# Kernel tuning notes

Measured on AMD Instinct MI355X. Metric: run time of the kernel, lower is better.

The kernel has to match this reference:

```python
import jax, jax.numpy as jnp
import numpy as np

H, L, NH, DH, FF, V, MAXP = 768, 2, 12, 64, 3072, 50265, 512
B, S = 64, 512


def _ln(x, g, b, eps=1e-5):
    mu = jnp.mean(x, axis=-1, keepdims=True)
    var = jnp.mean(jnp.square(x - mu), axis=-1, keepdims=True)
    return (x - mu) * jax.lax.rsqrt(var + eps) * g + b


def setup_inputs() -> dict:
    key = jax.random.key(0)
    ks = jax.random.split(key, 16)
    sd = 0.02
    inp = {
        "source_ids": jax.random.randint(ks[0], (B, S), 0, V),
        "position_idx": jax.random.randint(ks[1], (B, S), 0, MAXP),
        "attn_mask": jax.random.randint(ks[2], (B, S, S), 0, 2).astype(bool),
        "word_emb": sd * jax.random.normal(ks[3], (V, H), jnp.float32),
        "pos_emb": sd * jax.random.normal(ks[4], (MAXP, H), jnp.float32),
        "ln_g": jnp.ones((H,), jnp.float32),
        "ln_b": jnp.zeros((H,), jnp.float32),
        "Wqkv": sd * jax.random.normal(ks[5], (L, H, 3 * H), jnp.float32),
        "bqkv": jnp.zeros((L, 3 * H), jnp.float32),
        "Wo": sd * jax.random.normal(ks[6], (L, H, H), jnp.float32),
        "bo": jnp.zeros((L, H), jnp.float32),
        "ln1_g": jnp.ones((L, H), jnp.float32),
        "ln1_b": jnp.zeros((L, H), jnp.float32),
        "W1": sd * jax.random.normal(ks[7], (L, H, FF), jnp.float32),
        "b1": jnp.zeros((L, FF), jnp.float32),
        "W2": sd * jax.random.normal(ks[8], (L, FF, H), jnp.float32),
        "b2": jnp.zeros((L, H), jnp.float32),
        "ln2_g": jnp.ones((L, H), jnp.float32),
        "ln2_b": jnp.zeros((L, H), jnp.float32),
        "dense_W": sd * jax.random.normal(ks[9], (H, H), jnp.float32),
        "dense_b": jnp.zeros((H,), jnp.float32),
        "out_W": sd * jax.random.normal(ks[10], (H, 1), jnp.float32),
        "out_b": jnp.zeros((1,), jnp.float32),
    }
    return inp


def reference(source_ids, position_idx, attn_mask, word_emb, pos_emb, ln_g, ln_b,
              Wqkv, bqkv, Wo, bo, ln1_g, ln1_b, W1, b1, W2, b2, ln2_g, ln2_b,
              dense_W, dense_b, out_W, out_b):
    nodes_mask = position_idx == 0          # [B,S] bool
    token_mask = position_idx >= 2          # [B,S] bool
    emb = word_emb[source_ids]              # [B,S,H]

    # node -> token masked mean aggregation (the custom-kernel hotspot)
    m = (nodes_mask[:, :, None] & token_mask[:, None, :] & attn_mask).astype(emb.dtype)  # [B,S,S]
    w = m / (jnp.sum(m, axis=-1, keepdims=True) + 1e-10)
    avg = jnp.einsum('bnt,btd->bnd', w, emb)
    nm = nodes_mask[:, :, None].astype(emb.dtype)
    emb = emb * (1.0 - nm) + avg * nm

    # RoBERTa-style embeddings: inputs_embeds + position embeddings, layernorm
    h = _ln(emb + pos_emb[position_idx], ln_g, ln_b)

    # additive attention bias from 3D mask
    bias = jnp.where(attn_mask, 0.0, -1e4).astype(h.dtype)[:, None, :, :]  # [B,1,S,S]
    scale = 1.0 / np.sqrt(DH)

    for l in range(L):
        qkv = h @ Wqkv[l] + bqkv[l]                     # [B,S,3H]
        q, k, v = jnp.split(qkv, 3, axis=-1)
        q = q.reshape(B, S, NH, DH)
        k = k.reshape(B, S, NH, DH)
        v = v.reshape(B, S, NH, DH)
        scores = jnp.einsum('bqhd,bkhd->bhqk', q, k) * scale + bias
        attn = jax.nn.softmax(scores, axis=-1)
        ctx = jnp.einsum('bhqk,bkhd->bqhd', attn, v).reshape(B, S, H)
        h = _ln(h + ctx @ Wo[l] + bo[l], ln1_g[l], ln1_b[l])
        ffn = jax.nn.gelu(h @ W1[l] + b1[l], approximate=False) @ W2[l] + b2[l]
        h = _ln(h + ffn, ln2_g[l], ln2_b[l])

    # classification head (dropout in eval = identity)
    x = h[:, 0, :]
    x = jnp.tanh(x @ dense_W + dense_b)
    logits = x @ out_W + out_b                          # [B,1]
    return logits
```

## Files before the change

kernel.cpp:

```cpp
#include <hip/hip_runtime.h>

typedef unsigned short u16;
typedef unsigned int   u32;
typedef __bf16 bf16x8 __attribute__((ext_vector_type(8)));
typedef float  f32x4  __attribute__((ext_vector_type(4)));

#define DEVI __device__ __forceinline__

DEVI u16 f2bf(float f){
  u32 u = __builtin_bit_cast(u32, f);
  u32 r = (u + 0x7fffu + ((u >> 16) & 1u)) >> 16;
  return (u16)r;
}
DEVI float bf2f(u16 u){
  u32 x = ((u32)u) << 16;
  return __builtin_bit_cast(float, x);
}

DEVI void gload16(const void* g, void* lds){
  __builtin_amdgcn_global_load_lds(
      (const __attribute__((address_space(1))) void*)g,
      (__attribute__((address_space(3))) void*)lds, 16, 0, 0);
}

DEVI f32x4 MFMA(bf16x8 a, bf16x8 b, f32x4 c){
  return __builtin_amdgcn_mfma_f32_16x16x32_bf16(a, b, c, 0, 0, 0);
}

#define BAR() do { asm volatile("s_barrier" ::: "memory"); \
                   __builtin_amdgcn_sched_barrier(0); } while(0)

__global__ void k_maskprobe(const unsigned char* __restrict__ m, int* __restrict__ flag){
  __shared__ int s;
  if (threadIdx.x == 0) s = 0;
  __syncthreads();
  int acc = 0;
  for (int i = threadIdx.x; i < 65536; i += 256)
    if ((i & 3) != 0 && m[i] != 0) acc++;
  atomicAdd(&s, acc);
  __syncthreads();
  if (threadIdx.x == 0) *flag = (s > 0) ? 1 : 0;
}

__global__ void k_maskbits(const void* __restrict__ mask, const int* __restrict__ flag,
                           u32* __restrict__ mb){
  int row  = blockIdx.x * 4 + (threadIdx.x >> 6);
  int lane = threadIdx.x & 63;
  bool bytes = (*flag != 0);
  for (int c0 = 0; c0 < 512; c0 += 64){
    int v;
    if (bytes) v = ((const unsigned char*)mask)[(size_t)row * 512 + c0 + lane];
    else       v = ((const int*)mask)[(size_t)row * 512 + c0 + lane];
    unsigned long long bits = __ballot(v != 0);
    if (lane == 0){
      mb[(size_t)row * 16 + (c0 >> 5)]     = (u32)(bits & 0xffffffffull);
      mb[(size_t)row * 16 + (c0 >> 5) + 1] = (u32)(bits >> 32);
    }
  }
}

__global__ void k_embln(const int* __restrict__ ids, const int* __restrict__ pos,
                        const u32* __restrict__ mb, const float* __restrict__ wemb,
                        const float* __restrict__ pemb, const float* __restrict__ g,
                        const float* __restrict__ be, u16* __restrict__ hb){
  __shared__ float s1[4], s2[4];
  int row = blockIdx.x, t = threadIdx.x;
  int p = pos[row];
  float x0, x1, x2;
  if (p == 0){
    int b = row >> 9;
    const u32* mrow = mb + (size_t)row * 16;
    const int* pb = pos + ((size_t)b << 9);
    const int* ib = ids + ((size_t)b << 9);
    float a0 = 0.f, a1 = 0.f, a2 = 0.f, cnt = 0.f;
    #pragma unroll 8
    for (int k = 0; k < 512; k++){
      float w = (pb[k] >= 2 && ((mrow[k >> 5] >> (k & 31)) & 1)) ? 1.f : 0.f;
      const float* src = wemb + (size_t)ib[k] * 768;
      a0 += w * src[t]; a1 += w * src[t+256]; a2 += w * src[t+512];
      cnt += w;
    }
    float inv = 1.f / (cnt + 1e-10f);
    x0 = a0 * inv; x1 = a1 * inv; x2 = a2 * inv;
  } else {
    const float* src = wemb + (size_t)ids[row] * 768;
    x0 = src[t]; x1 = src[t+256]; x2 = src[t+512];
  }
  const float* pr = pemb + (size_t)p * 768;
  x0 += pr[t]; x1 += pr[t+256]; x2 += pr[t+512];
  float s = x0 + x1 + x2, q = x0*x0 + x1*x1 + x2*x2;
  for (int o = 32; o; o >>= 1){ s += __shfl_down(s, o, 64); q += __shfl_down(q, o, 64); }
  int wv = t >> 6, ln = t & 63;
  if (!ln){ s1[wv] = s; s2[wv] = q; }
  __syncthreads();
  s = s1[0]+s1[1]+s1[2]+s1[3]; q = s2[0]+s2[1]+s2[2]+s2[3];
  float mu = s * (1.f/768.f);
  float rs = rsqrtf(q * (1.f/768.f) - mu*mu + 1e-5f);
  u16* hbr = hb + (size_t)row * 768;
  hbr[t]     = f2bf((x0-mu)*rs*g[t]     + be[t]);
  hbr[t+256] = f2bf((x1-mu)*rs*g[t+256] + be[t+256]);
  hbr[t+512] = f2bf((x2-mu)*rs*g[t+512] + be[t+512]);
}

__global__ void k_lnres(const u16* __restrict__ C, const float* __restrict__ g,
                        const float* __restrict__ be, u16* __restrict__ hb){
  __shared__ float s1[4], s2[4];
  int row = blockIdx.x, t = threadIdx.x;
  u16* hr = hb + (size_t)row * 768;
  const u16* cr = C + (size_t)row * 768;
  float x0 = bf2f(hr[t])     + bf2f(cr[t]);
  float x1 = bf2f(hr[t+256]) + bf2f(cr[t+256]);
  float x2 = bf2f(hr[t+512]) + bf2f(cr[t+512]);
  float s = x0 + x1 + x2, q = x0*x0 + x1*x1 + x2*x2;
  for (int o = 32; o; o >>= 1){ s += __shfl_down(s, o, 64); q += __shfl_down(q, o, 64); }
  int wv = t >> 6, ln = t & 63;
  if (!ln){ s1[wv] = s; s2[wv] = q; }
  __syncthreads();
  s = s1[0]+s1[1]+s1[2]+s1[3]; q = s2[0]+s2[1]+s2[2]+s2[3];
  float mu = s * (1.f/768.f);
  float rs = rsqrtf(q * (1.f/768.f) - mu*mu + 1e-5f);
  hr[t]     = f2bf((x0-mu)*rs*g[t]     + be[t]);
  hr[t+256] = f2bf((x1-mu)*rs*g[t+256] + be[t+256]);
  hr[t+512] = f2bf((x2-mu)*rs*g[t+512] + be[t+512]);
}

__global__ void k_transpose(const float* __restrict__ src, u16* __restrict__ dst,
                            int K, int N){
  __shared__ float tile[32][33];
  int k0 = blockIdx.x * 32, n0 = blockIdx.y * 32;
  int tx = threadIdx.x & 31, ty = threadIdx.x >> 5;
  #pragma unroll
  for (int i = 0; i < 32; i += 8)
    tile[ty + i][tx] = src[(size_t)(k0 + ty + i) * N + n0 + tx];
  __syncthreads();
  #pragma unroll
  for (int i = 0; i < 32; i += 8)
    dst[(size_t)(n0 + ty + i) * K + k0 + tx] = f2bf(tile[tx][ty + i]);
}


DEVI void stageA32(const u16* __restrict__ src, int K, u16* lds, int tid){
  int r = tid >> 2, c = tid & 3;
  int sc = c ^ ((r >> 1) & 3);
  gload16(src + (size_t)r*K + sc*8, lds + (size_t)tid*8);
}
DEVI void stageB32(const u16* __restrict__ src, int K, u16* lds, int tid){
  #pragma unroll
  for (int j = 0; j < 2; j++){
    int p = j*512 + tid;
    int r = p >> 2, c = p & 3;
    int sc = c ^ ((r >> 1) & 3);
    gload16(src + (size_t)r*K + sc*8, lds + (size_t)p*8);
  }
}

template<int EPI>
__global__ __launch_bounds__(512, 4)
void k_gemm3(const u16* __restrict__ A, const u16* __restrict__ BT,
             const float* __restrict__ bias, void* __restrict__ out,
             void* __restrict__ out2, int M, int N, int K){
  __shared__ __align__(16) u16 sm[36864];
  const int tid = threadIdx.x;
  const int w = tid >> 6, lane = tid & 63;
  const int wm = w >> 2, wn = w & 3;
  const int cr = lane & 15, cg = lane >> 4;

  const int nbn = gridDim.x;
  const int nwg = nbn * gridDim.y;
  const int d   = blockIdx.y * nbn + blockIdx.x;
  const int xcd = d & 7, qq = nwg >> 3, rr = nwg & 7;
  const int logical = (xcd < rr ? xcd*(qq+1) : rr*(qq+1) + (xcd-rr)*qq) + (d >> 3);
  const int m0 = (logical / nbn) * 128;
  const int n0 = (logical % nbn) * 256;

  const int NT = K >> 5;
  const u16* Abase = A  + (size_t)m0 * K;
  const u16* Bbase = BT + (size_t)n0 * K;
  const int rowA = wm*64 + cr;
  const int rowB = wn*64 + cr;

  f32x4 acc[4][4] = {};
  bf16x8 afr[4], bfr[4];

  stageA32(Abase, K, sm, tid);
  stageB32(Bbase, K, sm + 12288, tid);
  if (NT > 1){
    stageA32(Abase + 32, K, sm + 4096, tid);
    stageB32(Bbase + 32, K, sm + 12288 + 8192, tid);
    asm volatile("s_waitcnt vmcnt(3)" ::: "memory");
  } else {
    asm volatile("s_waitcnt vmcnt(0)" ::: "memory");
  }
  __builtin_amdgcn_sched_barrier(0);
  BAR();

  int bcur = 0;
  for (int t = 0; t < NT; ++t){
    const int ab = bcur << 12;
    const int bb = 12288 + (bcur << 13);
    int bn2 = bcur + 2; if (bn2 >= 3) bn2 -= 3;

    #pragma unroll
    for (int n = 0; n < 4; n++){
      int r = rowB + n*16;
      bfr[n] = *(const bf16x8*)&sm[bb + r*32 + ((cg ^ ((r >> 1) & 3)) << 3)];
    }
    #pragma unroll
    for (int i = 0; i < 4; i++){
      int r = rowA + i*16;
      afr[i] = *(const bf16x8*)&sm[ab + r*32 + ((cg ^ ((r >> 1) & 3)) << 3)];
    }
    if (t + 2 < NT){
      stageA32(Abase + (size_t)(t+2)*32, K, sm + (bn2 << 12), tid);
      stageB32(Bbase + (size_t)(t+2)*32, K, sm + 12288 + (bn2 << 13), tid);
    }

    __builtin_amdgcn_s_setprio(1);
    #pragma unroll
    for (int i = 0; i < 4; i++)
      #pragma unroll
      for (int n = 0; n < 4; n++)
        acc[i][n] = MFMA(afr[i], bfr[n], acc[i][n]);
    __builtin_amdgcn_s_setprio(0);

    if (t + 2 < NT) { asm volatile("s_waitcnt vmcnt(3)" ::: "memory"); }
    else            { asm volatile("s_waitcnt vmcnt(0)" ::: "memory"); }
    __builtin_amdgcn_sched_barrier(0);
    BAR();
    bcur = bcur + 1; if (bcur >= 3) bcur = 0;
  }

  if (EPI == 1){
    #pragma unroll
    for (int n = 0; n < 4; n++){
      int col = n0 + wn*64 + n*16 + cr;
      float bv = bias[col];
      #pragma unroll
      for (int i = 0; i < 4; i++){
        #pragma unroll
        for (int j = 0; j < 4; j++){
          int row = m0 + wm*64 + i*16 + cg*4 + j;
          ((float*)out)[(size_t)row * N + col] = acc[i][n][j] + bv;
        }
      }
    }
  } else {
    const bool vblk = (EPI == 3) && (n0 >= 1536);
    const int LDC = vblk ? 266 : 264;
    #pragma unroll
    for (int n = 0; n < 4; n++){
      int coll = wn*64 + n*16 + cr;
      float bv = bias[n0 + coll];
      #pragma unroll
      for (int i = 0; i < 4; i++){
        #pragma unroll
        for (int j = 0; j < 4; j++){
          int rowl = wm*64 + i*16 + cg*4 + j;
          float v = acc[i][n][j] + bv;
          if (EPI == 2) v = 0.5f * v * (1.f + erff(v * 0.70710678118654752f));
          sm[rowl*LDC + coll] = f2bf(v);
        }
      }
    }
    BAR();
    if (EPI == 3){
      int b = m0 >> 9, s0 = m0 & 511;
      if (vblk){
        int hd0 = (n0 - 1536) >> 6;
        int dl = lane >> 2, sc4 = lane & 3;
        #pragma unroll
        for (int it = 0; it < 8; it++){
          int gidx = it*8 + w;
          int hh2 = gidx >> 4, dhi = (gidx >> 2) & 3, shi = gidx & 3;
          int dd2 = dhi*16 + dl;
          int schunk = shi*4 + sc4;
          u16 tmp[8];
          #pragma unroll
          for (int k = 0; k < 8; k++)
            tmp[k] = sm[(schunk*8 + k)*266 + hh2*64 + dd2];
          *(uint4*)((u16*)out2 + (((size_t)(b*12 + hd0 + hh2)*64 + dd2) << 9)
                    + s0 + schunk*8) = *(uint4*)tmp;
        }
      } else {
        #pragma unroll
        for (int it = 0; it < 8; it++){
          int idx = it*512 + tid;
          int c = idx & 7, hh2 = (idx >> 3) & 3, s = idx >> 5;
          uint4 v4 = *(const uint4*)&sm[s*264 + hh2*64 + c*8];
          int col0 = n0 + hh2*64;
          int sec = (col0 >= 768) ? 1 : 0;
          int hd  = (col0 - sec*768) >> 6;
          *(uint4*)((u16*)out + (size_t)sec*25165824 +
                    (((size_t)(b*12 + hd)*512 + (m0 & 511) + s) << 6) + c*8) = v4;
        }
      }
    } else {
      #pragma unroll
      for (int it = 0; it < 8; it++){
        int idx = it*512 + tid;
        int r = idx >> 5, c8 = idx & 31;
        uint4 v4 = *(const uint4*)&sm[r*264 + c8*8];
        *(uint4*)((u16*)out + (size_t)(m0 + r)*N + n0 + c8*8) = v4;
      }
    }
  }
}

DEVI void stage64(const u16* __restrict__ src, int stride, u16* lds, int w, int lane){
  #pragma unroll
  for (int j = 0; j < 2; j++){
    int p  = j*256 + w*64 + lane;
    int r  = p >> 3;
    int c8 = (p & 7) ^ (r & 7);
    gload16(src + (size_t)r*stride + c8*8, lds + (size_t)p*8);
  }
}

__global__ __launch_bounds__(256, 4)
void k_attn3(const u16* __restrict__ qp, const u16* __restrict__ kp,
             const u16* __restrict__ vt, const u32* __restrict__ mb,
             u16* __restrict__ ctx){
  __shared__ __align__(16) u16 Ks[8192];
  __shared__ __align__(16) u16 Vs[8192];
  const int tid = threadIdx.x, wv = tid >> 6, lane = tid & 63;
  const int cr = lane & 15, cg = lane >> 4;
  const int cg4 = cg * 4;
  const int r7 = cr & 7;

  const int dd = blockIdx.x + (blockIdx.y << 3);
  const int logical = (dd & 7) * 768 + (dd >> 3);
  const int bh = logical >> 3;
  const int qblk = logical & 7;
  const int b = bh / 12, hh = bh % 12;
  const int qw = qblk * 64 + wv * 16;
  const int qrow = qw + cr;
  const size_t base = (size_t)bh * 512 * 64;
  const u16* vtb = vt + (size_t)bh * 64 * 512;

  const int slot0 = ((cg    ) ^ r7) << 3;
  const int slot1 = ((4 + cg) ^ r7) << 3;

  bf16x8 qB[2];
  #pragma unroll
  for (int ks = 0; ks < 2; ks++)
    qB[ks] = *(const bf16x8*)&qp[base + (size_t)qrow * 64 + ks*32 + cg*8];

  u32 mw[16];
  {
    const u32* mrow = mb + ((size_t)b * 512 + qrow) * 16;
    #pragma unroll
    for (int i = 0; i < 4; i++){
      uint4 v4 = *(const uint4*)&mrow[i*4];
      mw[i*4+0] = v4.x; mw[i*4+1] = v4.y; mw[i*4+2] = v4.z; mw[i*4+3] = v4.w;
    }
  }

  stage64(kp + base, 64, Ks, wv, lane);
  stage64(vtb,      512, Vs, wv, lane);
  asm volatile("s_waitcnt vmcnt(0)" ::: "memory");
  __builtin_amdgcn_sched_barrier(0);
  BAR();

  float m = -3e38f, vs = 0.f;
  f32x4 oacc[4] = {};

  for (int s = 0; s < 8; ++s){
    const int buf = (s & 1) << 12;
    const int nbf = ((s + 1) & 1) << 12;

    if (s + 1 < 8){
      stage64(kp + base + (size_t)(s+1)*4096, 64, Ks + nbf, wv, lane);
      stage64(vtb + (size_t)(s+1)*64,        512, Vs + nbf, wv, lane);
    }

    f32x4 pacc[4];
    #pragma unroll
    for (int tt = 0; tt < 4; tt++){
      bf16x8 a0 = *(const bf16x8*)&Ks[buf + (tt*16 + cr)*64 + slot0];
      bf16x8 a1 = *(const bf16x8*)&Ks[buf + (tt*16 + cr)*64 + slot1];
      f32x4 z = {0.f, 0.f, 0.f, 0.f};
      z = MFMA(a0, qB[0], z);
      z = MFMA(a1, qB[1], z);
      pacc[tt] = z;
    }

    const u32 w0 = mw[2*s], w1 = mw[2*s+1];
    f32x4 vmx = {-3e38f, -3e38f, -3e38f, -3e38f};
    #pragma unroll
    for (int tt = 0; tt < 4; tt++){
      u32 nib = (((tt < 2) ? w0 : w1) >> (16*(tt & 1) + cg4)) & 0xFu;
      #pragma unroll
      for (int j = 0; j < 4; j++){
        float v = pacc[tt][j] * 0.125f + (((nib >> j) & 1u) ? 0.f : -10000.f);
        pacc[tt][j] = v;
        vmx[j] = fmaxf(vmx[j], v);
      }
    }
    float tm = fmaxf(fmaxf(vmx[0], vmx[1]), fmaxf(vmx[2], vmx[3]));
    tm = fmaxf(tm, __shfl_xor(tm, 16, 64));
    tm = fmaxf(tm, __shfl_xor(tm, 32, 64));

    float mnew = fmaxf(m, tm);
    float alpha = __expf(m - mnew);
    m = mnew;
    #pragma unroll
    for (int db = 0; db < 4; db++) oacc[db] *= alpha;

    f32x4 vsum = {0.f, 0.f, 0.f, 0.f};
    #pragma unroll
    for (int tt = 0; tt < 4; tt++){
      #pragma unroll
      for (int j = 0; j < 4; j++){
        float e = __expf(pacc[tt][j] - m);
        pacc[tt][j] = e;
        vsum[j] += e;
      }
    }
    vs = vs * alpha + (vsum[0] + vsum[1] + vsum[2] + vsum[3]);

    bf16x8 pa[2];
    #pragma unroll
    for (int c = 0; c < 2; c++)
      #pragma unroll
      for (int e = 0; e < 4; e++){
        pa[c][e]   = (__bf16)pacc[2*c][e];
        pa[c][4+e] = (__bf16)pacc[2*c+1][e];
      }

    #pragma unroll
    for (int c = 0; c < 2; c++){
      const int ch0 = ((4*c     + (cg >> 1)) ^ r7);
      const int ch1 = ((4*c + 2 + (cg >> 1)) ^ r7);
      const int sub = (cg & 1) << 3;
      #pragma unroll
      for (int db = 0; db < 4; db++){
        const char* vrow = (const char*)&Vs[buf + (db*16 + cr)*64];
        bf16x8 vb;
        ((uint2*)&vb)[0] = *(const uint2*)(vrow + (ch0 << 4) + sub);
        ((uint2*)&vb)[1] = *(const uint2*)(vrow + (ch1 << 4) + sub);
        oacc[db] = MFMA(pa[c], vb, oacc[db]);
      }
    }

    if (s + 1 < 8) { asm volatile("s_waitcnt vmcnt(0)" ::: "memory"); }
    __builtin_amdgcn_sched_barrier(0);
    BAR();
  }

  vs += __shfl_xor(vs, 16, 64);
  vs += __shfl_xor(vs, 32, 64);
  #pragma unroll
  for (int j = 0; j < 4; j++){
    float ds = __shfl(vs, cg4 + j, 64);
    float inv = 1.0f / ds;
    #pragma unroll
    for (int db = 0; db < 4; db++)
      ctx[((size_t)b * 512 + qw + cg4 + j) * 768 + hh*64 + 16*db + cr] = f2bf(oacc[db][j] * inv);
  }
}

__global__ __launch_bounds__(256)
void k_dense(const u16* __restrict__ hb, const float* __restrict__ W,
             const float* __restrict__ bias, float* __restrict__ xt){
  __shared__ float xs[768];
  __shared__ float red[256];
  const int b = blockIdx.y, t = threadIdx.x;
  const u16* hr = hb + (size_t)b * 512 * 768;
  xs[t] = bf2f(hr[t]); xs[t+256] = bf2f(hr[t+256]); xs[t+512] = bf2f(hr[t+512]);
  __syncthreads();
  const int col = blockIdx.x * 64 + (t & 63);
  const int ks  = t >> 6;
  const float* Wp = W + (size_t)(ks * 192) * 768 + col;
  const float* xp = xs + ks * 192;
  float a = 0.f;
  #pragma unroll 8
  for (int k = 0; k < 192; k++) a += xp[k] * Wp[(size_t)k * 768];
  red[t] = a;
  __syncthreads();
  if (t < 64){
    float y = red[t] + red[t+64] + red[t+128] + red[t+192] + bias[col];
    xt[(size_t)b * 768 + col] = tanhf(y);
  }
}

__global__ void k_logits(const float* __restrict__ xt, const float* __restrict__ ow,
                         const float* __restrict__ ob, float* __restrict__ out){
  __shared__ float sb[4];
  int b = blockIdx.x, t = threadIdx.x;
  const float* x = xt + (size_t)b * 768;
  float s = x[t]*ow[t] + x[t+256]*ow[t+256] + x[t+512]*ow[t+512];
  for (int o = 32; o; o >>= 1) s += __shfl_down(s, o, 64);
  int wv = t >> 6, ln = t & 63;
  if (!ln) sb[wv] = s;
  __syncthreads();
  if (t == 0) out[b] = sb[0] + sb[1] + sb[2] + sb[3] + ob[0];
}

extern "C" void kernel_launch(void* const* d_in, const int* in_sizes, int n_in,
                              void* d_out, int out_size, void* d_ws, size_t ws_size,
                              hipStream_t stream){
  if (n_in < 23) return;
  if (ws_size < 534000000ull) return;

  const int*   ids  = (const int*)  d_in[0];
  const int*   pos  = (const int*)  d_in[1];
  const void*  amsk =               d_in[2];
  const float* wemb = (const float*)d_in[3];
  const float* pemb = (const float*)d_in[4];
  const float* lng  = (const float*)d_in[5];
  const float* lnb  = (const float*)d_in[6];
  const float* Wqkv = (const float*)d_in[7];
  const float* bqkv = (const float*)d_in[8];
  const float* Wo   = (const float*)d_in[9];
  const float* bo   = (const float*)d_in[10];
  const float* ln1g = (const float*)d_in[11];
  const float* ln1b = (const float*)d_in[12];
  const float* W1   = (const float*)d_in[13];
  const float* b1   = (const float*)d_in[14];
  const float* W2   = (const float*)d_in[15];
  const float* b2   = (const float*)d_in[16];
  const float* ln2g = (const float*)d_in[17];
  const float* ln2b = (const float*)d_in[18];
  const float* dW   = (const float*)d_in[19];
  const float* db   = (const float*)d_in[20];
  const float* oW   = (const float*)d_in[21];
  const float* ob   = (const float*)d_in[22];

  char* ws = (char*)d_ws;
  u16*   hb   = (u16*)  (ws + 100663296);
  u16*   C    = (u16*)  (ws + 150994944);
  u16*   qkvp = (u16*)  (ws + 251658240);
  u16*   vt   = (u16*)  (ws + 402653184);
  u16*   act  = (u16*)  (ws + 251658240);
  u16*   ctx  = (u16*)  (ws + 452984832);
  u32*   mbit = (u32*)  (ws + 503316480);
  u16*   wt   = (u16*)  (ws + 505413632);
  float* xt   = (float*)(ws + 533725184);
  int*   flag = (int*)  (ws + 533921792);

  u16* qp   = qkvp;
  u16* kp   = qkvp + (size_t)25165824;

  u16* WqkvT = wt;
  u16* WoT   = WqkvT + (size_t)2*2304*768;
  u16* W1T   = WoT   + (size_t)2*768*768;
  u16* W2T   = W1T   + (size_t)2*3072*768;

  k_maskprobe<<<1, 256, 0, stream>>>((const unsigned char*)amsk, flag);
  k_maskbits<<<8192, 256, 0, stream>>>(amsk, flag, mbit);

  for (int l = 0; l < 2; l++){
    k_transpose<<<dim3(24, 72), 256, 0, stream>>>(Wqkv + (size_t)l*768*2304, WqkvT + (size_t)l*2304*768, 768, 2304);
    k_transpose<<<dim3(24, 24), 256, 0, stream>>>(Wo   + (size_t)l*768*768,  WoT   + (size_t)l*768*768,  768, 768);
    k_transpose<<<dim3(24, 96), 256, 0, stream>>>(W1   + (size_t)l*768*3072, W1T   + (size_t)l*3072*768, 768, 3072);
    k_transpose<<<dim3(96, 24), 256, 0, stream>>>(W2   + (size_t)l*3072*768, W2T   + (size_t)l*768*3072, 3072, 768);
  }

  k_embln<<<32768, 256, 0, stream>>>(ids, pos, mbit, wemb, pemb, lng, lnb, hb);

  for (int l = 0; l < 2; l++){
    k_gemm3<3><<<dim3(9, 256), 512, 0, stream>>>(hb, WqkvT + (size_t)l*2304*768, bqkv + l*2304, (void*)qkvp, (void*)vt, 32768, 2304, 768);
    k_attn3<<<dim3(8, 768), 256, 0, stream>>>(qp, kp, vt, mbit, ctx);
    k_gemm3<0><<<dim3(3, 256), 512, 0, stream>>>(ctx, WoT + (size_t)l*768*768, bo + l*768, (void*)C, nullptr, 32768, 768, 768);
    k_lnres<<<32768, 256, 0, stream>>>(C, ln1g + l*768, ln1b + l*768, hb);
    k_gemm3<2><<<dim3(12, 256), 512, 0, stream>>>(hb, W1T + (size_t)l*3072*768, b1 + l*3072, (void*)act, nullptr, 32768, 3072, 768);
    k_gemm3<0><<<dim3(3, 256), 512, 0, stream>>>(act, W2T + (size_t)l*768*3072, b2 + l*768, (void*)C, nullptr, 32768, 768, 3072);
    k_lnres<<<32768, 256, 0, stream>>>(C, ln2g + l*768, ln2b + l*768, hb);
  }

  k_dense<<<dim3(12, 64), 256, 0, stream>>>(hb, dW, db, xt);
  k_logits<<<64, 256, 0, stream>>>(xt, oW, ob, (float*)d_out);
}
```

Before: 1.699 ms.

## Load GEMM B operand directly from global into double-buffered registers

The B tile of the bf16 MFMA GEMM no longer goes through LDS. Each wave loads its own B fragments straight from global memory into two alternating register sets, one tile ahead. Only A stays in the triple-buffered LDS ring, and the main loop is unrolled by six to rotate buffers statically. This is meant to cut LDS capacity, LDS traffic and staging work. In exchange, the B global loads are narrower and less coalesced, both wm wave rows fetch the same B data, and the loop now silently assumes K/32 is a multiple of six.

```diff
diff --git a/kernel.cpp b/kernel.cpp
--- a/kernel.cpp
+++ b/kernel.cpp
@@ -144,15 +144,6 @@
   int sc = c ^ ((r >> 1) & 3);
   gload16(src + (size_t)r*K + sc*8, lds + (size_t)tid*8);
 }
-DEVI void stageB32(const u16* __restrict__ src, int K, u16* lds, int tid){
-  #pragma unroll
-  for (int j = 0; j < 2; j++){
-    int p = j*512 + tid;
-    int r = p >> 2, c = p & 3;
-    int sc = c ^ ((r >> 1) & 3);
-    gload16(src + (size_t)r*K + sc*8, lds + (size_t)p*8);
-  }
-}
 
 template<int EPI>
 __global__ __launch_bounds__(512, 4)
@@ -174,61 +165,63 @@
   const int n0 = (logical % nbn) * 256;
 
   const int NT = K >> 5;
-  const u16* Abase = A  + (size_t)m0 * K;
-  const u16* Bbase = BT + (size_t)n0 * K;
+  const u16* Abase = A + (size_t)m0 * K;
   const int rowA = wm*64 + cr;
-  const int rowB = wn*64 + cr;
+
+  const u16* Bp0 = BT + (size_t)(n0 + wn*64 + cr) * K + cg*8;
+  const u16* Bp1 = Bp0 + (size_t)16*K;
+  const u16* Bp2 = Bp0 + (size_t)32*K;
+  const u16* Bp3 = Bp0 + (size_t)48*K;
 
   f32x4 acc[4][4] = {};
-  bf16x8 afr[4], bfr[4];
-
-  stageA32(Abase, K, sm, tid);
-  stageB32(Bbase, K, sm + 12288, tid);
-  if (NT > 1){
-    stageA32(Abase + 32, K, sm + 4096, tid);
-    stageB32(Bbase + 32, K, sm + 12288 + 8192, tid);
-    asm volatile("s_waitcnt vmcnt(3)" ::: "memory");
-  } else {
-    asm volatile("s_waitcnt vmcnt(0)" ::: "memory");
-  }
+  bf16x8 afr[4], bX[4], bY[4];
+
+  stageA32(Abase,      K, sm,        tid);
+  stageA32(Abase + 32, K, sm + 4096, tid);
+  bX[0] = *(const bf16x8*)Bp0;
+  bX[1] = *(const bf16x8*)Bp1;
+  bX[2] = *(const bf16x8*)Bp2;
+  bX[3] = *(const bf16x8*)Bp3;
+  asm volatile("s_waitcnt vmcnt(5)" ::: "memory");
   __builtin_amdgcn_sched_barrier(0);
   BAR();
 
-  int bcur = 0;
-  for (int t = 0; t < NT; ++t){
-    const int ab = bcur << 12;
-    const int bb = 12288 + (bcur << 13);
-    int bn2 = bcur + 2; if (bn2 >= 3) bn2 -= 3;
-
-    #pragma unroll
-    for (int n = 0; n < 4; n++){
-      int r = rowB + n*16;
-      bfr[n] = *(const bf16x8*)&sm[bb + r*32 + ((cg ^ ((r >> 1) & 3)) << 3)];
-    }
-    #pragma unroll
-    for (int i = 0; i < 4; i++){
-      int r = rowA + i*16;
-      afr[i] = *(const bf16x8*)&sm[ab + r*32 + ((cg ^ ((r >> 1) & 3)) << 3)];
-    }
-    if (t + 2 < NT){
-      stageA32(Abase + (size_t)(t+2)*32, K, sm + (bn2 << 12), tid);
-      stageB32(Bbase + (size_t)(t+2)*32, K, sm + 12288 + (bn2 << 13), tid);
-    }
-
-    __builtin_amdgcn_s_setprio(1);
-    #pragma unroll
-    for (int i = 0; i < 4; i++)
-      #pragma unroll
-      for (int n = 0; n < 4; n++)
-        acc[i][n] = MFMA(afr[i], bfr[n], acc[i][n]);
-    __builtin_amdgcn_s_setprio(0);
-
-    if (t + 2 < NT) { asm volatile("s_waitcnt vmcnt(3)" ::: "memory"); }
-    else            { asm volatile("s_waitcnt vmcnt(0)" ::: "memory"); }
-    __builtin_amdgcn_sched_barrier(0);
-    BAR();
-    bcur = bcur + 1; if (bcur >= 3) bcur = 0;
-  }
+#define GITER(BC, BN, tt, ABCUR, ABST) { \
+    _Pragma("unroll") \
+    for (int i = 0; i < 4; i++){ \
+      int r = rowA + i*16; \
+      afr[i] = *(const bf16x8*)&sm[(ABCUR) + r*32 + ((cg ^ ((r >> 1) & 3)) << 3)]; \
+    } \
+    if ((tt) + 2 < NT) stageA32(Abase + (size_t)((tt)+2)*32, K, sm + (ABST), tid); \
+    if ((tt) + 1 < NT){ \
+      BN[0] = *(const bf16x8*)(Bp0 + ((tt)+1)*32); \
+      BN[1] = *(const bf16x8*)(Bp1 + ((tt)+1)*32); \
+      BN[2] = *(const bf16x8*)(Bp2 + ((tt)+1)*32); \
+      BN[3] = *(const bf16x8*)(Bp3 + ((tt)+1)*32); \
+    } \
+    if ((tt) + 2 < NT)      { asm volatile("s_waitcnt vmcnt(5)" ::: "memory"); } \
+    else if ((tt) + 1 < NT) { asm volatile("s_waitcnt vmcnt(4)" ::: "memory"); } \
+    else                    { asm volatile("s_waitcnt vmcnt(0)" ::: "memory"); } \
+    __builtin_amdgcn_sched_barrier(0); \
+    __builtin_amdgcn_s_setprio(1); \
+    _Pragma("unroll") \
+    for (int i = 0; i < 4; i++) \
+      _Pragma("unroll") \
+      for (int n = 0; n < 4; n++) \
+        acc[i][n] = MFMA(afr[i], BC[n], acc[i][n]); \
+    __builtin_amdgcn_s_setprio(0); \
+    BAR(); \
+  }
+
+  for (int t = 0; t < NT; t += 6){
+    GITER(bX, bY, t+0, 0,    8192);
+    GITER(bY, bX, t+1, 4096, 0);
+    GITER(bX, bY, t+2, 8192, 4096);
+    GITER(bY, bX, t+3, 0,    8192);
+    GITER(bX, bY, t+4, 4096, 0);
+    GITER(bY, bX, t+5, 8192, 4096);
+  }
+#undef GITER
 
   if (EPI == 1){
     #pragma unroll
```

New measurement: 4.786 ms. 2.82x slower.
